# Optimization experiments

Measured on AMD Instinct MI355X. Metric: run time of the kernel, lower is better.

## Reference

```python
import jax, jax.numpy as jnp
import numpy as np

NUM_HEADS = 12

def setup_inputs() -> dict:
    key = jax.random.key(0)
    ks = jax.random.split(key, 6)
    B, N, C = 8, 1024, 768
    s = 1.0 / np.sqrt(C).astype(np.float32)
    x = jax.random.normal(ks[0], (B, N, C), dtype=jnp.float32)
    Wq = jax.random.normal(ks[1], (C, C), dtype=jnp.float32) * s
    Wk = jax.random.normal(ks[2], (C, C), dtype=jnp.float32) * s
    Wv = jax.random.normal(ks[3], (C, C), dtype=jnp.float32) * s
    Wproj = jax.random.normal(ks[4], (C, C), dtype=jnp.float32) * s
    attn_bias = jax.random.normal(ks[5], (N, N), dtype=jnp.float32) * 0.02
    return {"x": x, "Wq": Wq, "Wk": Wk, "Wv": Wv, "Wproj": Wproj, "attn_bias": attn_bias}

def reference(x, Wq, Wk, Wv, Wproj, attn_bias):
    B, N, C = x.shape
    nh = NUM_HEADS
    d = C // nh                      # head_dim = qk_head_dim = 64
    scale = d ** -0.5
    # linear projections (bias=False), split heads: [B, nh, N, d]
    q = (x @ Wq).reshape(B, N, nh, d).transpose(0, 2, 1, 3) * scale
    k = (x @ Wk).reshape(B, N, nh, d).transpose(0, 2, 1, 3)
    v = (x @ Wv).reshape(B, N, nh, d).transpose(0, 2, 1, 3)
    # scores + learned additive bias (broadcast over B, nh), stable softmax
    scores = jnp.einsum('bhqd,bhkd->bhqk', q, k) + attn_bias
    attn = jax.nn.softmax(scores, axis=-1)       # [B, nh, N, N]
    out = jnp.einsum('bhqk,bhkd->bhqd', attn, v)
    out = out.transpose(0, 2, 1, 3).reshape(B, N, C) @ Wproj
    return out, attn
```

## Files before the change

kernel.cpp:

```cpp
#include <hip/hip_runtime.h>
#include <hip/hip_bf16.h>

typedef __bf16 bf16;
typedef __attribute__((ext_vector_type(4))) __bf16 bf16x4;
typedef __attribute__((ext_vector_type(8))) __bf16 bf16x8;
typedef __attribute__((ext_vector_type(4))) float f32x4;

#define MFMA(a,b,c) __builtin_amdgcn_mfma_f32_16x16x32_bf16(a,b,c,0,0,0)

__global__ __launch_bounds__(256) void convert_x_kernel(const float* __restrict__ x,
                                                        bf16* __restrict__ xb) {
    int i = blockIdx.x * 256 + threadIdx.x;
    float4 v = ((const float4*)x)[i];
    bf16x4 o = { (bf16)v.x, (bf16)v.y, (bf16)v.z, (bf16)v.w };
    ((bf16x4*)xb)[i] = o;
}

__global__ __launch_bounds__(1024) void convert_w_kernel(const float* __restrict__ W,
                                                         bf16* __restrict__ Wt) {
    __shared__ float tile[32][33];
    int k0 = blockIdx.x * 32, n0 = blockIdx.y * 32;
    int tx = threadIdx.x & 31, ty = threadIdx.x >> 5;
    tile[ty][tx] = W[(k0 + ty) * 768 + n0 + tx];
    __syncthreads();
    Wt[(n0 + ty) * 768 + k0 + tx] = (bf16)tile[tx][ty];
}

__global__ __launch_bounds__(256) void gemm_kernel(const bf16* __restrict__ A,
                                                   const bf16* __restrict__ Bt,
                                                   void* __restrict__ dst, int mode) {
    __shared__ bf16 As[64][40];
    __shared__ bf16 Bs[64][40];
    const int K = 768;
    int m0 = blockIdx.x * 64, n0 = blockIdx.y * 64;
    int tid = threadIdx.x, lane = tid & 63, w = tid >> 6;
    int wr = w >> 1, wc = w & 1;
    int lrow = tid >> 2, lch = (tid & 3) * 8;
    int fr = lane & 15, fg = lane >> 4;
    f32x4 acc[2][2] = {};
    for (int k0 = 0; k0 < K; k0 += 32) {
        __syncthreads();
        *(bf16x8*)&As[lrow][lch] = *(const bf16x8*)&A[(size_t)(m0 + lrow) * K + k0 + lch];
        *(bf16x8*)&Bs[lrow][lch] = *(const bf16x8*)&Bt[(size_t)(n0 + lrow) * K + k0 + lch];
        __syncthreads();
        bf16x8 af[2], bfr[2];
        for (int i = 0; i < 2; i++) af[i]  = *(const bf16x8*)&As[wr*32 + i*16 + fr][fg*8];
        for (int j = 0; j < 2; j++) bfr[j] = *(const bf16x8*)&Bs[wc*32 + j*16 + fr][fg*8];
        for (int i = 0; i < 2; i++)
            for (int j = 0; j < 2; j++)
                acc[i][j] = MFMA(af[i], bfr[j], acc[i][j]);
    }
    for (int i = 0; i < 2; i++) for (int j = 0; j < 2; j++) for (int r = 0; r < 4; r++) {
        int grow = m0 + wr*32 + i*16 + fg*4 + r;
        int gcol = n0 + wc*32 + j*16 + fr;
        float v = acc[i][j][r];
        if (mode == 3) {
            ((float*)dst)[(size_t)grow * 768 + gcol] = v;
        } else {
            int b = grow >> 10, np = grow & 1023;
            int h = gcol >> 6, dd = gcol & 63;
            bf16* o = (bf16*)dst;
            if (mode == 0)      o[((size_t)(b*12 + h)*1024 + np)*64 + dd] = (bf16)(v * 0.125f);
            else if (mode == 1) o[((size_t)(b*12 + h)*1024 + np)*64 + dd] = (bf16)v;
            else                o[((size_t)(b*12 + h)*64 + dd)*1024 + np] = (bf16)v;
        }
    }
}

__device__ inline int saddr(int row, int col) {
    int chunk = (col >> 2) ^ (row & 7);
    return row * 1024 + chunk * 4 + (col & 3);
}

__global__ __launch_bounds__(256) void attn_kernel(const bf16* __restrict__ qb,
                                                   const bf16* __restrict__ kb,
                                                   const bf16* __restrict__ vt,
                                                   const float* __restrict__ bias,
                                                   float* __restrict__ attn,
                                                   bf16* __restrict__ Ob) {
    __shared__ float S[16 * 1024];
    int bh = blockIdx.x, q0 = blockIdx.y * 16;
    int tid = threadIdx.x, lane = tid & 63, w = tid >> 6;
    int fr = lane & 15, fg = lane >> 4;
    const bf16* qp = qb + (size_t)bh * 65536;
    const bf16* kp = kb + (size_t)bh * 65536;
    const bf16* vp = vt + (size_t)bh * 65536;
    bf16x8 qa0 = *(const bf16x8*)&qp[(q0 + fr) * 64 + fg * 8];
    bf16x8 qa1 = *(const bf16x8*)&qp[(q0 + fr) * 64 + 32 + fg * 8];
    for (int j = 0; j < 16; j++) {
        int key0 = w * 256 + j * 16;
        bf16x8 kb0 = *(const bf16x8*)&kp[(key0 + fr) * 64 + fg * 8];
        bf16x8 kb1 = *(const bf16x8*)&kp[(key0 + fr) * 64 + 32 + fg * 8];
        f32x4 acc = {};
        acc = MFMA(qa0, kb0, acc);
        acc = MFMA(qa1, kb1, acc);
        for (int r = 0; r < 4; r++) {
            int row = fg * 4 + r, key = key0 + fr;
            S[saddr(row, key)] = acc[r] + bias[(q0 + row) * 1024 + key];
        }
    }
    __syncthreads();
    for (int rr = 0; rr < 4; rr++) {
        int row = rr * 4 + w;
        float vals[16], mx = -1e30f;
        for (int i = 0; i < 16; i++) { vals[i] = S[saddr(row, i*64 + lane)]; mx = fmaxf(mx, vals[i]); }
        for (int off = 32; off; off >>= 1) mx = fmaxf(mx, __shfl_xor(mx, off));
        float sum = 0.f;
        for (int i = 0; i < 16; i++) { vals[i] = __expf(vals[i] - mx); sum += vals[i]; }
        for (int off = 32; off; off >>= 1) sum += __shfl_xor(sum, off);
        float rcp = 1.f / sum;
        float* arow = attn + ((size_t)bh * 1024 + q0 + row) * 1024;
        for (int i = 0; i < 16; i++) {
            float p = vals[i] * rcp;
            S[saddr(row, i*64 + lane)] = p;
            arow[i*64 + lane] = p;
        }
    }
    __syncthreads();
    f32x4 oacc = {};
    for (int kk = 0; kk < 32; kk++) {
        int c0 = kk * 32 + fg * 8;
        f32x4 p0 = *(f32x4*)&S[saddr(fr, c0)];
        f32x4 p1 = *(f32x4*)&S[saddr(fr, c0 + 4)];
        bf16x8 pa;
        pa[0]=(bf16)p0[0]; pa[1]=(bf16)p0[1]; pa[2]=(bf16)p0[2]; pa[3]=(bf16)p0[3];
        pa[4]=(bf16)p1[0]; pa[5]=(bf16)p1[1]; pa[6]=(bf16)p1[2]; pa[7]=(bf16)p1[3];
        bf16x8 vb = *(const bf16x8*)&vp[(w*16 + fr) * 1024 + kk*32 + fg*8];
        oacc = MFMA(pa, vb, oacc);
    }
    int b = bh / 12, h = bh % 12;
    for (int r = 0; r < 4; r++) {
        int row = fg * 4 + r;
        Ob[((size_t)b * 1024 + q0 + row) * 768 + h * 64 + w * 16 + fr] = (bf16)oacc[r];
    }
}

extern "C" void kernel_launch(void* const* d_in, const int* in_sizes, int n_in,
                              void* d_out, int out_size, void* d_ws, size_t ws_size,
                              hipStream_t stream) {
    const float* x    = (const float*)d_in[0];
    const float* Wq   = (const float*)d_in[1];
    const float* Wk   = (const float*)d_in[2];
    const float* Wv   = (const float*)d_in[3];
    const float* Wp   = (const float*)d_in[4];
    const float* bias = (const float*)d_in[5];
    char* ws = (char*)d_ws;
    bf16* xb  = (bf16*)(ws + 0);
    bf16* wt  = (bf16*)(ws + 12582912);
    bf16* qbp = (bf16*)(ws + 17301504);
    bf16* kbp = (bf16*)(ws + 29884416);
    bf16* vtp = (bf16*)(ws + 42467328);
    bf16* obp = (bf16*)(ws + 55050240);
    float* out0 = (float*)d_out;
    float* attn = out0 + 6291456;

    convert_x_kernel<<<6144, 256, 0, stream>>>(x, xb);
    const float* Wsrc[4] = {Wq, Wk, Wv, Wp};
    for (int i = 0; i < 4; i++)
        convert_w_kernel<<<dim3(24,24), 1024, 0, stream>>>(Wsrc[i], wt + (size_t)i*589824);
    gemm_kernel<<<dim3(128,12), 256, 0, stream>>>(xb, wt + 0*589824, qbp, 0);
    gemm_kernel<<<dim3(128,12), 256, 0, stream>>>(xb, wt + 1*589824, kbp, 1);
    gemm_kernel<<<dim3(128,12), 256, 0, stream>>>(xb, wt + 2*589824, vtp, 2);
    attn_kernel<<<dim3(96,64), 256, 0, stream>>>(qbp, kbp, vtp, bias, attn, obp);
    gemm_kernel<<<dim3(128,12), 256, 0, stream>>>(obp, wt + 3*589824, out0, 3);
}
```

Before: 732.4 us.

## Enlarge GEMM tiles to 128x128 and keep attention scores in registers

```diff
diff --git a/kernel.cpp b/kernel.cpp
--- a/kernel.cpp
+++ b/kernel.cpp
@@ -29,30 +29,41 @@
 __global__ __launch_bounds__(256) void gemm_kernel(const bf16* __restrict__ A,
                                                    const bf16* __restrict__ Bt,
                                                    void* __restrict__ dst, int mode) {
-    __shared__ bf16 As[64][40];
-    __shared__ bf16 Bs[64][40];
+    __shared__ bf16 As[128][40];
+    __shared__ bf16 Bs[128][40];
     const int K = 768;
-    int m0 = blockIdx.x * 64, n0 = blockIdx.y * 64;
+    int m0 = blockIdx.x * 128, n0 = blockIdx.y * 128;
     int tid = threadIdx.x, lane = tid & 63, w = tid >> 6;
     int wr = w >> 1, wc = w & 1;
-    int lrow = tid >> 2, lch = (tid & 3) * 8;
     int fr = lane & 15, fg = lane >> 4;
-    f32x4 acc[2][2] = {};
+    int srow = tid >> 2, sch = (tid & 3) * 8;
+    f32x4 acc[4][4] = {};
     for (int k0 = 0; k0 < K; k0 += 32) {
         __syncthreads();
-        *(bf16x8*)&As[lrow][lch] = *(const bf16x8*)&A[(size_t)(m0 + lrow) * K + k0 + lch];
-        *(bf16x8*)&Bs[lrow][lch] = *(const bf16x8*)&Bt[(size_t)(n0 + lrow) * K + k0 + lch];
+        *(bf16x8*)&As[srow][sch]      = *(const bf16x8*)&A[(size_t)(m0 + srow) * K + k0 + sch];
+        *(bf16x8*)&As[srow + 64][sch] = *(const bf16x8*)&A[(size_t)(m0 + srow + 64) * K + k0 + sch];
+        *(bf16x8*)&Bs[srow][sch]      = *(const bf16x8*)&Bt[(size_t)(n0 + srow) * K + k0 + sch];
+        *(bf16x8*)&Bs[srow + 64][sch] = *(const bf16x8*)&Bt[(size_t)(n0 + srow + 64) * K + k0 + sch];
         __syncthreads();
-        bf16x8 af[2], bfr[2];
-        for (int i = 0; i < 2; i++) af[i]  = *(const bf16x8*)&As[wr*32 + i*16 + fr][fg*8];
-        for (int j = 0; j < 2; j++) bfr[j] = *(const bf16x8*)&Bs[wc*32 + j*16 + fr][fg*8];
-        for (int i = 0; i < 2; i++)
-            for (int j = 0; j < 2; j++)
+        bf16x8 af[4], bfr[4];
+        #pragma unroll
+        for (int i = 0; i < 4; i++) af[i]  = *(const bf16x8*)&As[wr*64 + i*16 + fr][fg*8];
+        #pragma unroll
+        for (int j = 0; j < 4; j++) bfr[j] = *(const bf16x8*)&Bs[wc*64 + j*16 + fr][fg*8];
+        #pragma unroll
+        for (int i = 0; i < 4; i++)
+            #pragma unroll
+            for (int j = 0; j < 4; j++)
                 acc[i][j] = MFMA(af[i], bfr[j], acc[i][j]);
     }
-    for (int i = 0; i < 2; i++) for (int j = 0; j < 2; j++) for (int r = 0; r < 4; r++) {
-        int grow = m0 + wr*32 + i*16 + fg*4 + r;
-        int gcol = n0 + wc*32 + j*16 + fr;
+    #pragma unroll
+    for (int i = 0; i < 4; i++)
+    #pragma unroll
+    for (int j = 0; j < 4; j++)
+    #pragma unroll
+    for (int r = 0; r < 4; r++) {
+        int grow = m0 + wr*64 + i*16 + fg*4 + r;
+        int gcol = n0 + wc*64 + j*16 + fr;
         float v = acc[i][j][r];
         if (mode == 3) {
             ((float*)dst)[(size_t)grow * 768 + gcol] = v;
@@ -67,18 +78,14 @@
     }
 }
 
-__device__ inline int saddr(int row, int col) {
-    int chunk = (col >> 2) ^ (row & 7);
-    return row * 1024 + chunk * 4 + (col & 3);
-}
-
 __global__ __launch_bounds__(256) void attn_kernel(const bf16* __restrict__ qb,
                                                    const bf16* __restrict__ kb,
                                                    const bf16* __restrict__ vt,
                                                    const float* __restrict__ bias,
                                                    float* __restrict__ attn,
                                                    bf16* __restrict__ Ob) {
-    __shared__ float S[16 * 1024];
+    __shared__ bf16 P[16 * 1024];
+    __shared__ float red[2][4][16];
     int bh = blockIdx.x, q0 = blockIdx.y * 16;
     int tid = threadIdx.x, lane = tid & 63, w = tid >> 6;
     int fr = lane & 15, fg = lane >> 4;
@@ -87,48 +94,62 @@
     const bf16* vp = vt + (size_t)bh * 65536;
     bf16x8 qa0 = *(const bf16x8*)&qp[(q0 + fr) * 64 + fg * 8];
     bf16x8 qa1 = *(const bf16x8*)&qp[(q0 + fr) * 64 + 32 + fg * 8];
+    f32x4 s[16];
+    #pragma unroll
     for (int j = 0; j < 16; j++) {
         int key0 = w * 256 + j * 16;
-        bf16x8 kb0 = *(const bf16x8*)&kp[(key0 + fr) * 64 + fg * 8];
-        bf16x8 kb1 = *(const bf16x8*)&kp[(key0 + fr) * 64 + 32 + fg * 8];
-        f32x4 acc = {};
-        acc = MFMA(qa0, kb0, acc);
-        acc = MFMA(qa1, kb1, acc);
-        for (int r = 0; r < 4; r++) {
-            int row = fg * 4 + r, key = key0 + fr;
-            S[saddr(row, key)] = acc[r] + bias[(q0 + row) * 1024 + key];
-        }
+        bf16x8 kf0 = *(const bf16x8*)&kp[(key0 + fr) * 64 + fg * 8];
+        bf16x8 kf1 = *(const bf16x8*)&kp[(key0 + fr) * 64 + 32 + fg * 8];
+        f32x4 a = {};
+        a = MFMA(kf0, qa0, a);
+        a = MFMA(kf1, qa1, a);
+        f32x4 bv = *(const f32x4*)&bias[(q0 + fr) * 1024 + key0 + fg * 4];
+        s[j] = a + bv;
     }
+    float mx = -1e30f;
+    #pragma unroll
+    for (int j = 0; j < 16; j++)
+        mx = fmaxf(fmaxf(fmaxf(mx, s[j][0]), fmaxf(s[j][1], s[j][2])), s[j][3]);
+    mx = fmaxf(mx, __shfl_xor(mx, 16));
+    mx = fmaxf(mx, __shfl_xor(mx, 32));
+    if (lane < 16) red[0][w][lane] = mx;
     __syncthreads();
-    for (int rr = 0; rr < 4; rr++) {
-        int row = rr * 4 + w;
-        float vals[16], mx = -1e30f;
-        for (int i = 0; i < 16; i++) { vals[i] = S[saddr(row, i*64 + lane)]; mx = fmaxf(mx, vals[i]); }
-        for (int off = 32; off; off >>= 1) mx = fmaxf(mx, __shfl_xor(mx, off));
-        float sum = 0.f;
-        for (int i = 0; i < 16; i++) { vals[i] = __expf(vals[i] - mx); sum += vals[i]; }
-        for (int off = 32; off; off >>= 1) sum += __shfl_xor(sum, off);
-        float rcp = 1.f / sum;
-        float* arow = attn + ((size_t)bh * 1024 + q0 + row) * 1024;
-        for (int i = 0; i < 16; i++) {
-            float p = vals[i] * rcp;
-            S[saddr(row, i*64 + lane)] = p;
-            arow[i*64 + lane] = p;
-        }
+    mx = fmaxf(fmaxf(red[0][0][fr], red[0][1][fr]), fmaxf(red[0][2][fr], red[0][3][fr]));
+    float sum = 0.f;
+    #pragma unroll
+    for (int j = 0; j < 16; j++) {
+        s[j][0] = __expf(s[j][0] - mx); s[j][1] = __expf(s[j][1] - mx);
+        s[j][2] = __expf(s[j][2] - mx); s[j][3] = __expf(s[j][3] - mx);
+        sum += s[j][0] + s[j][1] + s[j][2] + s[j][3];
+    }
+    sum += __shfl_xor(sum, 16);
+    sum += __shfl_xor(sum, 32);
+    if (lane < 16) red[1][w][lane] = sum;
+    __syncthreads();
+    float tot = (red[1][0][fr] + red[1][1][fr]) + (red[1][2][fr] + red[1][3][fr]);
+    float rcp = 1.f / tot;
+    float* arow = attn + ((size_t)bh * 1024 + q0 + fr) * 1024;
+    #pragma unroll
+    for (int j = 0; j < 16; j++) {
+        int key = w * 256 + j * 16 + fg * 4;
+        f32x4 p = s[j] * rcp;
+        *(f32x4*)&arow[key] = p;
+        bf16x4 pb = { (bf16)p[0], (bf16)p[1], (bf16)p[2], (bf16)p[3] };
+        int chunk = key >> 3;
+        *(bf16x4*)&P[fr * 1024 + ((chunk ^ (fr & 7)) << 3) + (key & 7)] = pb;
     }
     __syncthreads();
     f32x4 oacc = {};
+    #pragma unroll
     for (int kk = 0; kk < 32; kk++) {
-        int c0 = kk * 32 + fg * 8;
-        f32x4 p0 = *(f32x4*)&S[saddr(fr, c0)];
-        f32x4 p1 = *(f32x4*)&S[saddr(fr, c0 + 4)];
-        bf16x8 pa;
-        pa[0]=(bf16)p0[0]; pa[1]=(bf16)p0[1]; pa[2]=(bf16)p0[2]; pa[3]=(bf16)p0[3];
-        pa[4]=(bf16)p1[0]; pa[5]=(bf16)p1[1]; pa[6]=(bf16)p1[2]; pa[7]=(bf16)p1[3];
-        bf16x8 vb = *(const bf16x8*)&vp[(w*16 + fr) * 1024 + kk*32 + fg*8];
+        int k0e = kk * 32 + fg * 8;
+        int chunk = k0e >> 3;
+        bf16x8 pa = *(const bf16x8*)&P[fr * 1024 + ((chunk ^ (fr & 7)) << 3)];
+        bf16x8 vb = *(const bf16x8*)&vp[(w * 16 + fr) * 1024 + k0e];
         oacc = MFMA(pa, vb, oacc);
     }
     int b = bh / 12, h = bh % 12;
+    #pragma unroll
     for (int r = 0; r < 4; r++) {
         int row = fg * 4 + r;
         Ob[((size_t)b * 1024 + q0 + row) * 768 + h * 64 + w * 16 + fr] = (bf16)oacc[r];
@@ -158,9 +179,9 @@
     const float* Wsrc[4] = {Wq, Wk, Wv, Wp};
     for (int i = 0; i < 4; i++)
         convert_w_kernel<<<dim3(24,24), 1024, 0, stream>>>(Wsrc[i], wt + (size_t)i*589824);
-    gemm_kernel<<<dim3(128,12), 256, 0, stream>>>(xb, wt + 0*589824, qbp, 0);
-    gemm_kernel<<<dim3(128,12), 256, 0, stream>>>(xb, wt + 1*589824, kbp, 1);
-    gemm_kernel<<<dim3(128,12), 256, 0, stream>>>(xb, wt + 2*589824, vtp, 2);
+    gemm_kernel<<<dim3(64,6), 256, 0, stream>>>(xb, wt + 0*589824, qbp, 0);
+    gemm_kernel<<<dim3(64,6), 256, 0, stream>>>(xb, wt + 1*589824, kbp, 1);
+    gemm_kernel<<<dim3(64,6), 256, 0, stream>>>(xb, wt + 2*589824, vtp, 2);
     attn_kernel<<<dim3(96,64), 256, 0, stream>>>(qbp, kbp, vtp, bias, attn, obp);
-    gemm_kernel<<<dim3(128,12), 256, 0, stream>>>(obp, wt + 3*589824, out0, 3);
+    gemm_kernel<<<dim3(64,6), 256, 0, stream>>>(obp, wt + 3*589824, out0, 3);
 }
```

New measurement: 773.3 us. 1.06x slower.
